# Optimization experiments

Hardware: AMD Instinct MI355X
Metric: run time of the kernel (lower is better)

The kernel has to match this reference:

```python
import jax, jax.numpy as jnp
import numpy as np

D_MODEL = 128
NUM_LAYERS = 2
D_FF = 512
VOCAB = 128
OUT_DIM = 10
B, S = 512, 256
EPS_FEAT = 1e-6
LN_EPS = 1e-5


def _pos_encoding(seq_len, d):
    pos = jnp.arange(seq_len, dtype=jnp.float32)[:, None]            # [S,1]
    div = jnp.exp(jnp.arange(0, d, 2, dtype=jnp.float32) * (-np.log(10000.0) / d))
    ang = pos * div                                                   # [S,D/2]
    pe = jnp.stack([jnp.sin(ang), jnp.cos(ang)], axis=-1).reshape(seq_len, d)
    return pe[:, None, :]                                             # [S,1,D]


def _layer_norm(x, g, b):
    mu = jnp.mean(x, axis=-1, keepdims=True)
    var = jnp.mean(jnp.square(x - mu), axis=-1, keepdims=True)
    return (x - mu) * jax.lax.rsqrt(var + LN_EPS) * g + b


def setup_inputs() -> dict:
    key = jax.random.key(0)
    ks = jax.random.split(key, 20)
    sc = 0.02
    inp = {
        'src': jax.random.randint(ks[0], (B, S), 0, VOCAB),
        'emb': jax.random.normal(ks[1], (VOCAB, D_MODEL), jnp.float32) * sc,
        'wq': jax.random.normal(ks[2], (NUM_LAYERS, D_MODEL, D_MODEL), jnp.float32) * sc,
        'bq': jnp.zeros((NUM_LAYERS, D_MODEL), jnp.float32),
        'wk': jax.random.normal(ks[3], (NUM_LAYERS, D_MODEL, D_MODEL), jnp.float32) * sc,
        'bk': jnp.zeros((NUM_LAYERS, D_MODEL), jnp.float32),
        'wv': jax.random.normal(ks[4], (NUM_LAYERS, D_MODEL, D_MODEL), jnp.float32) * sc,
        'bv': jnp.zeros((NUM_LAYERS, D_MODEL), jnp.float32),
        'w1': jax.random.normal(ks[5], (NUM_LAYERS, D_FF, D_MODEL), jnp.float32) * sc,
        'b1': jnp.zeros((NUM_LAYERS, D_FF), jnp.float32),
        'w2': jax.random.normal(ks[6], (NUM_LAYERS, D_MODEL, D_FF), jnp.float32) * sc,
        'b2': jnp.zeros((NUM_LAYERS, D_MODEL), jnp.float32),
        'g1': jnp.ones((NUM_LAYERS, D_MODEL), jnp.float32),
        'beta1': jnp.zeros((NUM_LAYERS, D_MODEL), jnp.float32),
        'g2': jnp.ones((NUM_LAYERS, D_MODEL), jnp.float32),
        'beta2': jnp.zeros((NUM_LAYERS, D_MODEL), jnp.float32),
        'fc_w': jax.random.normal(ks[7], (OUT_DIM, D_MODEL), jnp.float32) * sc,
        'fc_b': jnp.zeros((OUT_DIM,), jnp.float32),
    }
    return inp


def reference(src, emb, wq, bq, wk, bk, wv, bv, w1, b1, w2, b2,
              g1, beta1, g2, beta2, fc_w, fc_b):
    # src: [B,S] int -> permute -> [S,B]
    x = emb[src.T] * np.sqrt(float(D_MODEL))          # [S,B,D]
    x = x + _pos_encoding(x.shape[0], D_MODEL)
    for l in range(NUM_LAYERS):
        # Linear attention (faithful to original: einsum 'b' axis = seq here)
        Q = jax.nn.relu(jnp.einsum('sbd,ed->sbe', x, wq[l]) + bq[l]) + EPS_FEAT
        K = jax.nn.relu(jnp.einsum('sbd,ed->sbe', x, wk[l]) + bk[l]) + EPS_FEAT
        V = jnp.einsum('sbd,ed->sbe', x, wv[l]) + bv[l]
        KV = jnp.einsum('snd,sne->sde', K, V)         # [S,D,D] (n = batch axis)
        Z = 1.0 / (jnp.einsum('snd,sd->sn', Q, K.sum(axis=1)) + EPS_FEAT)  # [S,B]
        attn = jnp.einsum('snd,sde,sn->sne', Q, KV, Z)  # [S,B,D]
        x = _layer_norm(x + attn, g1[l], beta1[l])
        ff = jnp.einsum('sbf,df->sbd',
                        jax.nn.relu(jnp.einsum('sbd,fd->sbf', x, w1[l]) + b1[l]),
                        w2[l]) + b2[l]
        x = _layer_norm(x + ff, g2[l], beta2[l])
    x = jnp.transpose(x, (1, 0, 2))                   # [B,S,D]
    pooled = jnp.mean(x, axis=1)                      # [B,D]
    return pooled @ fc_w.T + fc_b                     # [B,OUT]
```

## Files before the change

kernel.cpp:

```cpp
#include <hip/hip_runtime.h>

typedef unsigned short u16;
typedef unsigned int u32;
typedef short bf16x8 __attribute__((ext_vector_type(8)));
typedef float f32x4 __attribute__((ext_vector_type(4)));

__device__ __forceinline__ float b2f(u16 v) { return __uint_as_float(((u32)v) << 16); }
__device__ __forceinline__ u16 f2b(float f) {
    u32 x = __float_as_uint(f);
    return (u16)((x + 0x7fffu + ((x >> 16) & 1u)) >> 16);
}

__device__ __forceinline__ void gld_lds16(const u16* g, u16* l) {
    __builtin_amdgcn_global_load_lds(
        (const __attribute__((address_space(1))) unsigned int*)g,
        (__attribute__((address_space(3))) unsigned int*)l,
        16, 0, 0);
}

#define S_LEN 256
#define B_SZ  512
#define DM    128
#define DFF   512
#define MROWS (S_LEN * B_SZ)

__device__ __forceinline__ int sw16(int r, int d) {
    return r * 128 + ((((d >> 3) ^ (r & 15)) & 15) << 3) + (d & 7);
}

__global__ __launch_bounds__(256) void detect_kernel(const u32* __restrict__ embw,
                                                     int* __restrict__ flag) {
    int z = 0, big = 0;
    for (int i = threadIdx.x; i < 8192; i += 256) {
        u32 w = embw[i];
        u32 lo = w & 0xffffu;
        if (lo == 0u) z++;
        else if (((lo >> 7) & 0xffu) >= 0xC0u) big++;
    }
#pragma unroll
    for (int off = 32; off > 0; off >>= 1) {
        z   += __shfl_xor(z, off, 64);
        big += __shfl_xor(big, off, 64);
    }
    __shared__ int zz[4], bb[4];
    if ((threadIdx.x & 63) == 0) { zz[threadIdx.x >> 6] = z; bb[threadIdx.x >> 6] = big; }
    __syncthreads();
    if (threadIdx.x == 0) {
        int Z = zz[0] + zz[1] + zz[2] + zz[3];
        int Bc = bb[0] + bb[1] + bb[2] + bb[3];
        flag[0] = (Z > 4096 || Bc > 16) ? 1 : 0;
    }
}

struct Ptrs { const void* p[17]; };

__global__ __launch_bounds__(256) void convert_kernel(Ptrs ps, u16* __restrict__ canon,
                                                      const int* __restrict__ flag) {
    const int cnt[17] = {16384,32768,256,32768,256,32768,256,131072,1024,131072,
                         256,256,256,256,256,1280,10};
    const int off[17] = {0,16384,49152,49408,82176,82432,115200,115456,246528,
                         247552,378624,378880,379136,379392,379648,379904,381184};
    const int bst[18] = {0,8,24,25,41,42,58,59,123,124,188,189,190,191,192,193,194,195};
    const int isf = *flag;
    const int blk = blockIdx.x;
    int idx = 0;
#pragma unroll
    for (int i = 0; i < 17; ++i) if (blk >= bst[i + 1]) idx = i + 1;
    const int local = blk - bst[idx];
    const int n = cnt[idx];
    const void* sp = ps.p[idx];
    u16* dp = canon + off[idx];
#pragma unroll
    for (int j = 0; j < 8; ++j) {
        int e = local * 2048 + j * 256 + threadIdx.x;
        if (e < n) {
            u16 v = isf ? f2b(((const float*)sp)[e]) : ((const u16*)sp)[e];
            dp[e] = v;
        }
    }
}

__global__ __launch_bounds__(256) void pe_kernel(float* __restrict__ PE) {
    int idx = blockIdx.x * 256 + threadIdx.x;
    int s = idx >> 6, d2 = idx & 63;
    float ang = (float)s * expf((float)(d2 * 2) * -0.0719557841560639f);
    float2 sc; sc.x = sinf(ang); sc.y = cosf(ang);
    *(float2*)(PE + s * DM + d2 * 2) = sc;
}

__global__ __launch_bounds__(256) void embed_kernel(const int* __restrict__ src,
                                                    const u16* __restrict__ emb,
                                                    const float* __restrict__ PE,
                                                    u16* __restrict__ X) {
    int idx = blockIdx.x * 256 + threadIdx.x;
    int dq = idx & 15;
    int m = idx >> 4;
    int s = m >> 9;
    int b = m & 511;
    int tok = src[b * S_LEN + s];
    int d = dq * 8;
    uint4 ev = *(const uint4*)(emb + tok * DM + d);
    const float* pe = PE + s * DM + d;
    u16 o[8];
    const u32 ew[4] = {ev.x, ev.y, ev.z, ev.w};
#pragma unroll
    for (int p = 0; p < 4; ++p) {
        float e0 = __uint_as_float((ew[p] & 0xffffu) << 16) * 11.3137084989847604f;
        float e1 = __uint_as_float(ew[p] & 0xffff0000u)     * 11.3137084989847604f;
        o[p * 2]     = f2b(e0 + pe[p * 2]);
        o[p * 2 + 1] = f2b(e1 + pe[p * 2 + 1]);
    }
    uint4 wv;
    wv.x = (u32)o[0] | ((u32)o[1] << 16);
    wv.y = (u32)o[2] | ((u32)o[3] << 16);
    wv.z = (u32)o[4] | ((u32)o[5] << 16);
    wv.w = (u32)o[6] | ((u32)o[7] << 16);
    *(uint4*)(X + (size_t)m * DM + d) = wv;
}

__global__ __launch_bounds__(256) void kvproj_kernel(
    const u16* __restrict__ X, const u16* __restrict__ Wk, const u16* __restrict__ bk,
    const u16* __restrict__ Wv, const u16* __restrict__ bv,
    u16* __restrict__ KVt, float* __restrict__ Ksum)
{
    __shared__ __align__(16) char sm_[49152];
    u16* Xs = (u16*)sm_;
    u16* Kt = (u16*)(sm_ + 16384);
    u16* Vt = (u16*)(sm_ + 32768);
    const int s = blockIdx.x, t = threadIdx.x;
    const int w = t >> 6, quad = (t >> 4) & 3, lr = t & 15;
    const int l = t & 63;
    const u16* Xg = X + (size_t)s * B_SZ * DM;

#define STAGE_XS(B0)                                                            \
    {                                                                           \
        _Pragma("unroll")                                                       \
        for (int i = 0; i < 4; ++i) {                                           \
            int r = w * 16 + i * 4 + (l >> 4);                                  \
            int ss = (l & 15) ^ (r & 15);                                       \
            gld_lds16(Xg + (size_t)((B0) + r) * DM + (ss << 3),                 \
                      Xs + w * 2048 + i * 512);                                 \
        }                                                                       \
    }

    bf16x8 wkf[2][4], wvf[2][4];
    float kb[2], vb[2];
#pragma unroll
    for (int ct = 0; ct < 2; ++ct) {
        int e = w * 32 + ct * 16 + lr;
#pragma unroll
        for (int kc = 0; kc < 4; ++kc) {
            wkf[ct][kc] = *(const bf16x8*)(Wk + e * 128 + kc * 32 + quad * 8);
            wvf[ct][kc] = *(const bf16x8*)(Wv + e * 128 + kc * 32 + quad * 8);
        }
        kb[ct] = b2f(bk[e]);
        vb[ct] = b2f(bv[e]);
    }

    const f32x4 z4 = {0.f, 0.f, 0.f, 0.f};
    f32x4 kvacc[2][8];
#pragma unroll
    for (int dt = 0; dt < 2; ++dt)
#pragma unroll
        for (int ct = 0; ct < 8; ++ct) kvacc[dt][ct] = z4;
    float ks[2] = {0.f, 0.f};

    STAGE_XS(0)
    __syncthreads();

    for (int b0 = 0; b0 < B_SZ; b0 += 64) {
        f32x4 pa[4][2];
#pragma unroll
        for (int mt = 0; mt < 4; ++mt) { pa[mt][0] = z4; pa[mt][1] = z4; }
#pragma unroll
        for (int kc = 0; kc < 4; ++kc) {
            bf16x8 a[4];
#pragma unroll
            for (int mt = 0; mt < 4; ++mt)
                a[mt] = *(const bf16x8*)(Xs + sw16(mt * 16 + lr, kc * 32 + quad * 8));
#pragma unroll
            for (int ct = 0; ct < 2; ++ct)
#pragma unroll
                for (int mt = 0; mt < 4; ++mt)
                    pa[mt][ct] = __builtin_amdgcn_mfma_f32_16x16x32_bf16(a[mt], wkf[ct][kc], pa[mt][ct], 0, 0, 0);
        }
#pragma unroll
        for (int ct = 0; ct < 2; ++ct) {
            int e = w * 32 + ct * 16 + lr, e7 = e & 7;
#pragma unroll
            for (int mt = 0; mt < 4; ++mt) {
                u16 h[4]; float ssum = 0.f;
#pragma unroll
                for (int j = 0; j < 4; ++j) {
                    float v = fmaxf(pa[mt][ct][j] + kb[ct], 0.f) + 1e-6f;
                    h[j] = f2b(v); ssum += b2f(h[j]);
                }
                ks[ct] += ssum;
                uint2 pk; pk.x = (u32)h[0] | ((u32)h[1] << 16); pk.y = (u32)h[2] | ((u32)h[3] << 16);
                int bs = mt * 2 + (quad >> 1);
                *(uint2*)(Kt + e * 64 + (((bs ^ e7) & 7) << 3) + (quad & 1) * 4) = pk;
            }
        }
#pragma unroll
        for (int mt = 0; mt < 4; ++mt) { pa[mt][0] = z4; pa[mt][1] = z4; }
#pragma unroll
        for (int kc = 0; kc < 4; ++kc) {
            bf16x8 a[4];
#pragma unroll
            for (int mt = 0; mt < 4; ++mt)
                a[mt] = *(const bf16x8*)(Xs + sw16(mt * 16 + lr, kc * 32 + quad * 8));
#pragma unroll
            for (int ct = 0; ct < 2; ++ct)
#pragma unroll
                for (int mt = 0; mt < 4; ++mt)
                    pa[mt][ct] = __builtin_amdgcn_mfma_f32_16x16x32_bf16(a[mt], wvf[ct][kc], pa[mt][ct], 0, 0, 0);
        }
#pragma unroll
        for (int ct = 0; ct < 2; ++ct) {
            int e = w * 32 + ct * 16 + lr, e7 = e & 7;
#pragma unroll
            for (int mt = 0; mt < 4; ++mt) {
                u16 h[4];
#pragma unroll
                for (int j = 0; j < 4; ++j) h[j] = f2b(pa[mt][ct][j] + vb[ct]);
                uint2 pk; pk.x = (u32)h[0] | ((u32)h[1] << 16); pk.y = (u32)h[2] | ((u32)h[3] << 16);
                int bs = mt * 2 + (quad >> 1);
                *(uint2*)(Vt + e * 64 + (((bs ^ e7) & 7) << 3) + (quad & 1) * 4) = pk;
            }
        }
        __syncthreads();
        if (b0 < B_SZ - 64) STAGE_XS(b0 + 64)
#pragma unroll
        for (int kc = 0; kc < 2; ++kc) {
            bf16x8 ka[2];
#pragma unroll
            for (int dt = 0; dt < 2; ++dt) {
                int d = (2 * w + dt) * 16 + lr;
                ka[dt] = *(const bf16x8*)(Kt + d * 64 + ((((kc * 4 + quad) ^ (d & 7)) & 7) << 3));
            }
#pragma unroll
            for (int ct = 0; ct < 8; ++ct) {
                int e = ct * 16 + lr;
                bf16x8 vf = *(const bf16x8*)(Vt + e * 64 + ((((kc * 4 + quad) ^ (e & 7)) & 7) << 3));
                kvacc[0][ct] = __builtin_amdgcn_mfma_f32_16x16x32_bf16(ka[0], vf, kvacc[0][ct], 0, 0, 0);
                kvacc[1][ct] = __builtin_amdgcn_mfma_f32_16x16x32_bf16(ka[1], vf, kvacc[1][ct], 0, 0, 0);
            }
        }
        __syncthreads();
    }
#undef STAGE_XS
#pragma unroll
    for (int ct = 0; ct < 2; ++ct) {
        float v = ks[ct];
        v += __shfl_xor(v, 16, 64);
        v += __shfl_xor(v, 32, 64);
        if (quad == 0) Ksum[s * 128 + w * 32 + ct * 16 + lr] = v;
    }
    u16* KVg = KVt + (size_t)s * (DM * DM);
#pragma unroll
    for (int dt = 0; dt < 2; ++dt) {
        int d0 = (2 * w + dt) * 16 + quad * 4;
#pragma unroll
        for (int ct = 0; ct < 8; ++ct) {
            int e = ct * 16 + lr;
            u16 h[4];
#pragma unroll
            for (int j = 0; j < 4; ++j) h[j] = f2b(kvacc[dt][ct][j]);
            uint2 pk; pk.x = (u32)h[0] | ((u32)h[1] << 16); pk.y = (u32)h[2] | ((u32)h[3] << 16);
            *(uint2*)(KVg + e * 128 + d0) = pk;
        }
    }
}

__global__ __launch_bounds__(256) void attn_ln_kernel(
    const u16* X, const u16* __restrict__ Wq, const u16* __restrict__ bq,
    const u16* __restrict__ KVt, const float* __restrict__ Ksum,
    u16* Xout, const u16* __restrict__ g, const u16* __restrict__ beta)
{
    __shared__ __align__(16) char sm_[65536];
    u16* R1 = (u16*)sm_;
    u16* R2 = (u16*)(sm_ + 32768);
    const int blk = blockIdx.x, s = blk >> 2, rc = blk & 3, t = threadIdx.x;
    const int w = t >> 6, quad = (t >> 4) & 3, lr = t & 15;
    const int l = t & 63;
    const size_t m0 = (size_t)s * B_SZ + rc * 128;

#pragma unroll
    for (int i = 0; i < 8; ++i) {
        int r = w * 32 + i * 4 + (l >> 4);
        int ss = (l & 15) ^ (r & 15);
        gld_lds16(Wq + (size_t)r * DM + (ss << 3), R1 + w * 4096 + i * 512);
        gld_lds16(X + (m0 + r) * DM + (ss << 3),   R2 + w * 4096 + i * 512);
    }
    __syncthreads();
    const f32x4 z4 = {0.f, 0.f, 0.f, 0.f};
    f32x4 qacc[2][8];
#pragma unroll
    for (int mt = 0; mt < 2; ++mt)
#pragma unroll
        for (int ct = 0; ct < 8; ++ct) qacc[mt][ct] = z4;
#pragma unroll
    for (int kc = 0; kc < 4; ++kc) {
        bf16x8 a[2];
#pragma unroll
        for (int mt = 0; mt < 2; ++mt)
            a[mt] = *(const bf16x8*)(R2 + sw16(w * 32 + mt * 16 + lr, kc * 32 + quad * 8));
#pragma unroll
        for (int ct = 0; ct < 8; ++ct) {
            bf16x8 wf = *(const bf16x8*)(R1 + sw16(ct * 16 + lr, kc * 32 + quad * 8));
            qacc[0][ct] = __builtin_amdgcn_mfma_f32_16x16x32_bf16(a[0], wf, qacc[0][ct], 0, 0, 0);
            qacc[1][ct] = __builtin_amdgcn_mfma_f32_16x16x32_bf16(a[1], wf, qacc[1][ct], 0, 0, 0);
        }
    }
    __syncthreads();
    const u16* KVg = KVt + (size_t)s * (DM * DM);
#pragma unroll
    for (int i = 0; i < 8; ++i) {
        int e = w * 32 + i * 4 + (l >> 4);
        int ss = (l & 15) ^ (e & 15);
        gld_lds16(KVg + (size_t)e * DM + (ss << 3), R2 + w * 4096 + i * 512);
    }
    float ksm[8], bqv[8];
#pragma unroll
    for (int ct = 0; ct < 8; ++ct) {
        ksm[ct] = Ksum[s * 128 + ct * 16 + lr];
        bqv[ct] = b2f(bq[ct * 16 + lr]);
    }
    float zden[2][4];
#pragma unroll
    for (int mt = 0; mt < 2; ++mt)
#pragma unroll
        for (int j = 0; j < 4; ++j) zden[mt][j] = 0.f;
#pragma unroll
    for (int mt = 0; mt < 2; ++mt)
#pragma unroll
        for (int ct = 0; ct < 8; ++ct) {
            int d = ct * 16 + lr;
#pragma unroll
            for (int j = 0; j < 4; ++j) {
                float qv = fmaxf(qacc[mt][ct][j] + bqv[ct], 0.f) + 1e-6f;
                u16 qb16 = f2b(qv);
                zden[mt][j] += b2f(qb16) * ksm[ct];
                int b = w * 32 + mt * 16 + quad * 4 + j;
                R1[sw16(b, d)] = qb16;
            }
        }
#pragma unroll
    for (int mt = 0; mt < 2; ++mt)
#pragma unroll
        for (int j = 0; j < 4; ++j) {
            float v = zden[mt][j];
            v += __shfl_xor(v, 1, 64); v += __shfl_xor(v, 2, 64);
            v += __shfl_xor(v, 4, 64); v += __shfl_xor(v, 8, 64);
            zden[mt][j] = 1.f / (v + 1e-6f);
        }
    __syncthreads();
    f32x4 oacc[2][8];
#pragma unroll
    for (int mt = 0; mt < 2; ++mt)
#pragma unroll
        for (int ct = 0; ct < 8; ++ct) oacc[mt][ct] = z4;
#pragma unroll
    for (int kc = 0; kc < 4; ++kc) {
        bf16x8 qa[2];
#pragma unroll
        for (int mt = 0; mt < 2; ++mt)
            qa[mt] = *(const bf16x8*)(R1 + sw16(w * 32 + mt * 16 + lr, kc * 32 + quad * 8));
#pragma unroll
        for (int ct = 0; ct < 8; ++ct) {
            bf16x8 kf = *(const bf16x8*)(R2 + sw16(ct * 16 + lr, kc * 32 + quad * 8));
            oacc[0][ct] = __builtin_amdgcn_mfma_f32_16x16x32_bf16(qa[0], kf, oacc[0][ct], 0, 0, 0);
            oacc[1][ct] = __builtin_amdgcn_mfma_f32_16x16x32_bf16(qa[1], kf, oacc[1][ct], 0, 0, 0);
        }
    }
    float gv[8], bev[8];
#pragma unroll
    for (int ct = 0; ct < 8; ++ct) {
        gv[ct]  = b2f(g[ct * 16 + lr]);
        bev[ct] = b2f(beta[ct * 16 + lr]);
    }
#pragma unroll
    for (int mt = 0; mt < 2; ++mt)
#pragma unroll
        for (int j = 0; j < 4; ++j) {
            int b = w * 32 + mt * 16 + quad * 4 + j;
            const u16* xr = X + (m0 + b) * DM;
            float vals[8], sum = 0.f, sq = 0.f;
#pragma unroll
            for (int ct = 0; ct < 8; ++ct) {
                float v = fmaf(oacc[mt][ct][j], zden[mt][j], b2f(xr[ct * 16 + lr]));
                vals[ct] = v; sum += v; sq += v * v;
            }
            sum += __shfl_xor(sum, 1, 64); sq += __shfl_xor(sq, 1, 64);
            sum += __shfl_xor(sum, 2, 64); sq += __shfl_xor(sq, 2, 64);
            sum += __shfl_xor(sum, 4, 64); sq += __shfl_xor(sq, 4, 64);
            sum += __shfl_xor(sum, 8, 64); sq += __shfl_xor(sq, 8, 64);
            float mean = sum * 0.0078125f;
            float var  = sq * 0.0078125f - mean * mean;
            float rstd = rsqrtf(fmaxf(var, 0.f) + 1e-5f);
            u16* xo = Xout + (m0 + b) * DM;
#pragma unroll
            for (int ct = 0; ct < 8; ++ct)
                xo[ct * 16 + lr] = f2b((vals[ct] - mean) * rstd * gv[ct] + bev[ct]);
        }
}

__global__ __launch_bounds__(256, 4) void mlp_kernel(
    const u16* X, const u16* __restrict__ W1, const u16* __restrict__ b1,
    const u16* __restrict__ W2, const u16* __restrict__ b2,
    u16* Xout, const u16* __restrict__ g, const u16* __restrict__ beta)
{
    __shared__ __align__(16) char sm_[40960];
    u16* W1c = (u16*)sm_;
    u16* W2c = (u16*)(sm_ + 16384);
    u16* Hc  = (u16*)(sm_ + 32768);
    const int t = threadIdx.x;
    const int m0 = blockIdx.x * 64;
    const int w  = t >> 6;
    const int quad = (t >> 4) & 3;
    const int lr = t & 15;
    const int l  = t & 63;

    bf16x8 af[4];
    {
        const u16* xr = X + (size_t)(m0 + w * 16 + lr) * DM + quad * 8;
#pragma unroll
        for (int kc = 0; kc < 4; ++kc)
            af[kc] = *(const bf16x8*)(xr + kc * 32);
    }

    const f32x4 zero4 = {0.f, 0.f, 0.f, 0.f};
    f32x4 zacc[8];
#pragma unroll
    for (int ct = 0; ct < 8; ++ct) zacc[ct] = zero4;

#define STAGE_CHUNK(FC)                                                         \
    {                                                                           \
        _Pragma("unroll")                                                       \
        for (int i = 0; i < 4; ++i) {                                           \
            int r = w * 16 + i * 4 + (l >> 4);                                  \
            int sslot = (l & 15) ^ (r & 15);                                    \
            gld_lds16(W1 + (size_t)((FC) + r) * DM + (sslot << 3),              \
                      W1c + w * 2048 + i * 512);                                \
        }                                                                       \
        _Pragma("unroll")                                                       \
        for (int i = 0; i < 4; ++i) {                                           \
            int d = w * 32 + i * 8 + (l >> 3);                                  \
            int sslot = (l & 7) ^ (d & 7);                                      \
            gld_lds16(W2 + (size_t)d * DFF + (FC) + (sslot << 3),               \
                      W2c + w * 2048 + i * 512);                                \
        }                                                                       \
    }

    STAGE_CHUNK(0)
    __syncthreads();

    for (int fc = 0; fc < DFF; fc += 64) {
        f32x4 hacc[4];
#pragma unroll
        for (int ct = 0; ct < 4; ++ct) hacc[ct] = zero4;
#pragma unroll
        for (int kc = 0; kc < 4; ++kc)
#pragma unroll
            for (int ct = 0; ct < 4; ++ct) {
                bf16x8 bf_ = *(const bf16x8*)(W1c + sw16(ct * 16 + lr, kc * 32 + quad * 8));
                hacc[ct] = __builtin_amdgcn_mfma_f32_16x16x32_bf16(af[kc], bf_, hacc[ct], 0, 0, 0);
            }
#pragma unroll
        for (int ct = 0; ct < 4; ++ct) {
            int f = ct * 16 + lr;
            float hbv = b2f(b1[fc + f]);
#pragma unroll
            for (int j = 0; j < 4; ++j) {
                int m = w * 16 + quad * 4 + j;
                float v = fmaxf(hacc[ct][j] + hbv, 0.f);
                Hc[m * 64 + ((((f >> 3) ^ (m & 7)) & 7) << 3) + (f & 7)] = f2b(v);
            }
        }
#pragma unroll
        for (int kc = 0; kc < 2; ++kc) {
            int m = w * 16 + lr;
            bf16x8 ha = *(const bf16x8*)(Hc + m * 64 + ((((kc * 4 + quad) ^ (m & 7)) & 7) << 3));
#pragma unroll
            for (int ct = 0; ct < 8; ++ct) {
                int d = ct * 16 + lr;
                bf16x8 wb = *(const bf16x8*)(W2c + d * 64 + ((((kc * 4 + quad) ^ (d & 7)) & 7) << 3));
                zacc[ct] = __builtin_amdgcn_mfma_f32_16x16x32_bf16(ha, wb, zacc[ct], 0, 0, 0);
            }
        }
        __syncthreads();
        if (fc < DFF - 64) {
            STAGE_CHUNK(fc + 64)
            __syncthreads();
        }
    }
#undef STAGE_CHUNK

    float gv[8], bev[8], bbv[8];
#pragma unroll
    for (int ct = 0; ct < 8; ++ct) {
        gv[ct]  = b2f(g[ct * 16 + lr]);
        bev[ct] = b2f(beta[ct * 16 + lr]);
        bbv[ct] = b2f(b2[ct * 16 + lr]);
    }
#pragma unroll
    for (int j = 0; j < 4; ++j) {
        int m = w * 16 + quad * 4 + j;
        const u16* xr = X + (size_t)(m0 + m) * DM;
        float vals[8], sum = 0.f, sq = 0.f;
#pragma unroll
        for (int ct = 0; ct < 8; ++ct) {
            float v = zacc[ct][j] + bbv[ct] + b2f(xr[ct * 16 + lr]);
            vals[ct] = v; sum += v; sq += v * v;
        }
        sum += __shfl_xor(sum, 1, 64); sq += __shfl_xor(sq, 1, 64);
        sum += __shfl_xor(sum, 2, 64); sq += __shfl_xor(sq, 2, 64);
        sum += __shfl_xor(sum, 4, 64); sq += __shfl_xor(sq, 4, 64);
        sum += __shfl_xor(sum, 8, 64); sq += __shfl_xor(sq, 8, 64);
        float mean = sum * 0.0078125f;
        float var  = sq * 0.0078125f - mean * mean;
        float rstd = rsqrtf(fmaxf(var, 0.f) + 1e-5f);
        u16* xo = Xout + (size_t)(m0 + m) * DM;
#pragma unroll
        for (int ct = 0; ct < 8; ++ct)
            xo[ct * 16 + lr] = f2b((vals[ct] - mean) * rstd * gv[ct] + bev[ct]);
    }
}

__global__ __launch_bounds__(128) void pool_fc_kernel(
    const u16* __restrict__ X, const u16* __restrict__ fcw,
    const u16* __restrict__ fcb, void* __restrict__ Out,
    const int* __restrict__ flag)
{
    __shared__ float pool[128];
    const int b = blockIdx.x, t = threadIdx.x;
    float acc = 0.f;
    for (int s = 0; s < S_LEN; ++s)
        acc += b2f(X[((size_t)s * B_SZ + b) * DM + t]);
    pool[t] = acc * (1.0f / 256.0f);
    __syncthreads();
    if (t < 10) {
        float o = b2f(fcb[t]);
        for (int d = 0; d < 128; ++d) o += pool[d] * b2f(fcw[t * 128 + d]);
        if (*flag) ((float*)Out)[b * 10 + t] = o;
        else       ((u16*)Out)[b * 10 + t] = f2b(o);
    }
}

extern "C" void kernel_launch(void* const* d_in, const int* in_sizes, int n_in,
                              void* d_out, int out_size, void* d_ws, size_t ws_size,
                              hipStream_t stream)
{
    const int* src = (const int*)d_in[0];

    char* ws = (char*)d_ws;
    u16*   X    = (u16*)ws;
    u16*   KVt  = (u16*)(ws + 33554432);
    float* Ksum = (float*)(ws + 41943040);
    int*   flag = (int*)(ws + 42074112);
    u16*   cn   = (u16*)(ws + 42074368);
    float* PE   = (float*)(ws + 33554432);

    u16* emb = cn + 0;
    u16* wq  = cn + 16384;
    u16* bq  = cn + 49152;
    u16* wk  = cn + 49408;
    u16* bk  = cn + 82176;
    u16* wv  = cn + 82432;
    u16* bvp = cn + 115200;
    u16* w1  = cn + 115456;
    u16* b1  = cn + 246528;
    u16* w2  = cn + 247552;
    u16* b2  = cn + 378624;
    u16* g1  = cn + 378880;
    u16* be1 = cn + 379136;
    u16* g2  = cn + 379392;
    u16* be2 = cn + 379648;
    u16* fcw = cn + 379904;
    u16* fcb = cn + 381184;

    detect_kernel<<<1, 256, 0, stream>>>((const u32*)d_in[1], flag);

    Ptrs ps;
    for (int i = 0; i < 17; ++i) ps.p[i] = d_in[i + 1];
    convert_kernel<<<195, 256, 0, stream>>>(ps, cn, flag);

    pe_kernel<<<64, 256, 0, stream>>>(PE);
    embed_kernel<<<MROWS * 16 / 256, 256, 0, stream>>>(src, emb, PE, X);

    for (int l = 0; l < 2; ++l) {
        kvproj_kernel<<<S_LEN, 256, 0, stream>>>(
            X, wk + l * DM * DM, bk + l * DM, wv + l * DM * DM, bvp + l * DM, KVt, Ksum);
        attn_ln_kernel<<<S_LEN * 4, 256, 0, stream>>>(
            X, wq + l * DM * DM, bq + l * DM, KVt, Ksum, X, g1 + l * DM, be1 + l * DM);
        mlp_kernel<<<MROWS / 64, 256, 0, stream>>>(
            X, w1 + l * DFF * DM, b1 + l * DFF, w2 + l * DM * DFF, b2 + l * DM,
            X, g2 + l * DM, be2 + l * DM);
    }

    pool_fc_kernel<<<B_SZ, 128, 0, stream>>>(X, fcw, fcb, d_out, flag);
}
```

Baseline: 366.8 us.

## Split KV projection across two blocks per position and alias MLP hidden buffer

```diff
diff --git a/kernel.cpp b/kernel.cpp
--- a/kernel.cpp
+++ b/kernel.cpp
@@ -123,11 +123,11 @@
     const u16* __restrict__ Wv, const u16* __restrict__ bv,
     u16* __restrict__ KVt, float* __restrict__ Ksum)
 {
-    __shared__ __align__(16) char sm_[49152];
+    __shared__ __align__(16) char sm_[40960];
     u16* Xs = (u16*)sm_;
     u16* Kt = (u16*)(sm_ + 16384);
     u16* Vt = (u16*)(sm_ + 32768);
-    const int s = blockIdx.x, t = threadIdx.x;
+    const int blk = blockIdx.x, s = blk >> 1, eh = blk & 1, t = threadIdx.x;
     const int w = t >> 6, quad = (t >> 4) & 3, lr = t & 15;
     const int l = t & 63;
     const u16* Xg = X + (size_t)s * B_SZ * DM;
@@ -143,26 +143,32 @@
         }                                                                       \
     }
 
-    bf16x8 wkf[2][4], wvf[2][4];
-    float kb[2], vb[2];
+    bf16x8 wkf[2][4];
+    float kb[2];
 #pragma unroll
     for (int ct = 0; ct < 2; ++ct) {
         int e = w * 32 + ct * 16 + lr;
 #pragma unroll
-        for (int kc = 0; kc < 4; ++kc) {
+        for (int kc = 0; kc < 4; ++kc)
             wkf[ct][kc] = *(const bf16x8*)(Wk + e * 128 + kc * 32 + quad * 8);
-            wvf[ct][kc] = *(const bf16x8*)(Wv + e * 128 + kc * 32 + quad * 8);
-        }
         kb[ct] = b2f(bk[e]);
-        vb[ct] = b2f(bv[e]);
+    }
+    bf16x8 wvf[4];
+    float vb1;
+    {
+        int eg = eh * 64 + w * 16 + lr;
+#pragma unroll
+        for (int kc = 0; kc < 4; ++kc)
+            wvf[kc] = *(const bf16x8*)(Wv + eg * 128 + kc * 32 + quad * 8);
+        vb1 = b2f(bv[eg]);
     }
 
     const f32x4 z4 = {0.f, 0.f, 0.f, 0.f};
-    f32x4 kvacc[2][8];
+    f32x4 kvacc[2][4];
 #pragma unroll
     for (int dt = 0; dt < 2; ++dt)
 #pragma unroll
-        for (int ct = 0; ct < 8; ++ct) kvacc[dt][ct] = z4;
+        for (int ct = 0; ct < 4; ++ct) kvacc[dt][ct] = z4;
     float ks[2] = {0.f, 0.f};
 
     STAGE_XS(0)
@@ -201,8 +207,9 @@
                 *(uint2*)(Kt + e * 64 + (((bs ^ e7) & 7) << 3) + (quad & 1) * 4) = pk;
             }
         }
-#pragma unroll
-        for (int mt = 0; mt < 4; ++mt) { pa[mt][0] = z4; pa[mt][1] = z4; }
+        f32x4 pv[4];
+#pragma unroll
+        for (int mt = 0; mt < 4; ++mt) pv[mt] = z4;
 #pragma unroll
         for (int kc = 0; kc < 4; ++kc) {
             bf16x8 a[4];
@@ -210,22 +217,19 @@
             for (int mt = 0; mt < 4; ++mt)
                 a[mt] = *(const bf16x8*)(Xs + sw16(mt * 16 + lr, kc * 32 + quad * 8));
 #pragma unroll
-            for (int ct = 0; ct < 2; ++ct)
-#pragma unroll
-                for (int mt = 0; mt < 4; ++mt)
-                    pa[mt][ct] = __builtin_amdgcn_mfma_f32_16x16x32_bf16(a[mt], wvf[ct][kc], pa[mt][ct], 0, 0, 0);
-        }
-#pragma unroll
-        for (int ct = 0; ct < 2; ++ct) {
-            int e = w * 32 + ct * 16 + lr, e7 = e & 7;
+            for (int mt = 0; mt < 4; ++mt)
+                pv[mt] = __builtin_amdgcn_mfma_f32_16x16x32_bf16(a[mt], wvf[kc], pv[mt], 0, 0, 0);
+        }
+        {
+            int el = w * 16 + lr, e7 = el & 7;
 #pragma unroll
             for (int mt = 0; mt < 4; ++mt) {
                 u16 h[4];
 #pragma unroll
-                for (int j = 0; j < 4; ++j) h[j] = f2b(pa[mt][ct][j] + vb[ct]);
+                for (int j = 0; j < 4; ++j) h[j] = f2b(pv[mt][j] + vb1);
                 uint2 pk; pk.x = (u32)h[0] | ((u32)h[1] << 16); pk.y = (u32)h[2] | ((u32)h[3] << 16);
                 int bs = mt * 2 + (quad >> 1);
-                *(uint2*)(Vt + e * 64 + (((bs ^ e7) & 7) << 3) + (quad & 1) * 4) = pk;
+                *(uint2*)(Vt + el * 64 + (((bs ^ e7) & 7) << 3) + (quad & 1) * 4) = pk;
             }
         }
         __syncthreads();
@@ -239,9 +243,9 @@
                 ka[dt] = *(const bf16x8*)(Kt + d * 64 + ((((kc * 4 + quad) ^ (d & 7)) & 7) << 3));
             }
 #pragma unroll
-            for (int ct = 0; ct < 8; ++ct) {
-                int e = ct * 16 + lr;
-                bf16x8 vf = *(const bf16x8*)(Vt + e * 64 + ((((kc * 4 + quad) ^ (e & 7)) & 7) << 3));
+            for (int ct = 0; ct < 4; ++ct) {
+                int el = ct * 16 + lr;
+                bf16x8 vf = *(const bf16x8*)(Vt + el * 64 + ((((kc * 4 + quad) ^ (el & 7)) & 7) << 3));
                 kvacc[0][ct] = __builtin_amdgcn_mfma_f32_16x16x32_bf16(ka[0], vf, kvacc[0][ct], 0, 0, 0);
                 kvacc[1][ct] = __builtin_amdgcn_mfma_f32_16x16x32_bf16(ka[1], vf, kvacc[1][ct], 0, 0, 0);
             }
@@ -254,20 +258,20 @@
         float v = ks[ct];
         v += __shfl_xor(v, 16, 64);
         v += __shfl_xor(v, 32, 64);
-        if (quad == 0) Ksum[s * 128 + w * 32 + ct * 16 + lr] = v;
+        if (quad == 0 && eh == 0) Ksum[s * 128 + w * 32 + ct * 16 + lr] = v;
     }
     u16* KVg = KVt + (size_t)s * (DM * DM);
 #pragma unroll
     for (int dt = 0; dt < 2; ++dt) {
         int d0 = (2 * w + dt) * 16 + quad * 4;
 #pragma unroll
-        for (int ct = 0; ct < 8; ++ct) {
-            int e = ct * 16 + lr;
+        for (int ct = 0; ct < 4; ++ct) {
+            int eg = eh * 64 + ct * 16 + lr;
             u16 h[4];
 #pragma unroll
             for (int j = 0; j < 4; ++j) h[j] = f2b(kvacc[dt][ct][j]);
             uint2 pk; pk.x = (u32)h[0] | ((u32)h[1] << 16); pk.y = (u32)h[2] | ((u32)h[3] << 16);
-            *(uint2*)(KVg + e * 128 + d0) = pk;
+            *(uint2*)(KVg + eg * 128 + d0) = pk;
         }
     }
 }
@@ -405,15 +409,15 @@
         }
 }
 
-__global__ __launch_bounds__(256, 4) void mlp_kernel(
+__global__ __launch_bounds__(256, 5) void mlp_kernel(
     const u16* X, const u16* __restrict__ W1, const u16* __restrict__ b1,
     const u16* __restrict__ W2, const u16* __restrict__ b2,
     u16* Xout, const u16* __restrict__ g, const u16* __restrict__ beta)
 {
-    __shared__ __align__(16) char sm_[40960];
+    __shared__ __align__(16) char sm_[32768];
     u16* W1c = (u16*)sm_;
     u16* W2c = (u16*)(sm_ + 16384);
-    u16* Hc  = (u16*)(sm_ + 32768);
+    u16* Hc  = (u16*)sm_;
     const int t = threadIdx.x;
     const int m0 = blockIdx.x * 64;
     const int w  = t >> 6;
@@ -466,6 +470,7 @@
                 bf16x8 bf_ = *(const bf16x8*)(W1c + sw16(ct * 16 + lr, kc * 32 + quad * 8));
                 hacc[ct] = __builtin_amdgcn_mfma_f32_16x16x32_bf16(af[kc], bf_, hacc[ct], 0, 0, 0);
             }
+        __syncthreads();
 #pragma unroll
         for (int ct = 0; ct < 4; ++ct) {
             int f = ct * 16 + lr;
@@ -589,7 +594,7 @@
     embed_kernel<<<MROWS * 16 / 256, 256, 0, stream>>>(src, emb, PE, X);
 
     for (int l = 0; l < 2; ++l) {
-        kvproj_kernel<<<S_LEN, 256, 0, stream>>>(
+        kvproj_kernel<<<S_LEN * 2, 256, 0, stream>>>(
             X, wk + l * DM * DM, bk + l * DM, wv + l * DM * DM, bvp + l * DM, KVt, Ksum);
         attn_ln_kernel<<<S_LEN * 4, 256, 0, stream>>>(
             X, wq + l * DM * DM, bq + l * DM, KVt, Ksum, X, g1 + l * DM, be1 + l * DM);
```

Result: slower. 473.0 us (+29.0%).
